# Kernel tuning notes

Hardware: AMD Instinct MI355X
Metric: run time of the kernel (lower is better)

## Reference

```python
import jax, jax.numpy as jnp
import numpy as np

B, N = 128, 64
HID, MLP, DS, DV = 128, 128, 32, 32
DH = MLP - DS - DV  # 64
FILL = -10.0


def _embed_mask(x, W, b, fill):
    # Linear+ReLU on non-NaN rows; fill NaN rows with `fill` (matches embed_with_masking).
    nan = jnp.isnan(x).any(-1)
    e = jax.nn.relu(jnp.where(jnp.isnan(x), 0.0, x) @ W + b)
    return jnp.where(nan[..., None], jnp.asarray(fill, x.dtype), e)


def setup_inputs() -> dict:
    key = jax.random.key(0)
    ks = jax.random.split(key, 12)
    s = 0.05
    return {
        "hidden_states": jax.random.normal(ks[0], (B, N, HID), jnp.float32),
        "obs1": jax.random.normal(ks[1], (B, N, 2), jnp.float32),
        "obs2": jax.random.normal(ks[2], (B, N, 2), jnp.float32),
        "w_sp": jax.random.normal(ks[3], (2, DS), jnp.float32) * s,
        "b_sp": jnp.zeros((DS,), jnp.float32),
        "w_vel": jax.random.normal(ks[4], (2, DV), jnp.float32) * s,
        "b_vel": jnp.zeros((DV,), jnp.float32),
        "w_hid": jax.random.normal(ks[5], (HID, DH), jnp.float32) * s,
        "b_hid": jnp.zeros((DH,), jnp.float32),
        "wq": jax.random.normal(ks[6], (MLP, MLP), jnp.float32) * s,
        "wk": jax.random.normal(ks[7], (MLP, MLP), jnp.float32) * s,
        "wv": jax.random.normal(ks[8], (MLP, MLP), jnp.float32) * s,
        "in_proj_w": jax.random.normal(ks[9], (MLP, 3 * MLP), jnp.float32) * s,
        "in_proj_b": jnp.zeros((3 * MLP,), jnp.float32),
        "mha_out_w": jax.random.normal(ks[10], (MLP, MLP), jnp.float32) * s,
        "mha_out_b": jnp.zeros((MLP,), jnp.float32),
        "out_w": jax.random.normal(ks[11], (MLP, MLP), jnp.float32) * s,
        "out_b": jnp.zeros((MLP,), jnp.float32),
    }


def reference(hidden_states, obs1, obs2, w_sp, b_sp, w_vel, b_vel, w_hid, b_hid,
              wq, wk, wv, in_proj_w, in_proj_b, mha_out_w, mha_out_b, out_w, out_b):
    b, n = obs2.shape[0], obs2.shape[1]
    # relative positions: rel[b,i,j] = obs2[b,j] - obs2[b,i]
    rel = obs2[:, None, :, :] - obs2[:, :, None, :]              # [B,N,N,2]
    sp = _embed_mask(rel, w_sp, b_sp, FILL)                      # [B,N,N,DS]
    hid = _embed_mask(hidden_states, w_hid, b_hid, 0.0)          # [B,N,DH]
    hid_unf = jnp.broadcast_to(hid[:, None, :, :], (b, n, n, DH))
    vel = obs2 - obs1
    relvel = vel[:, None, :, :] - vel[:, :, None, :]             # [B,N,N,2]
    dv = _embed_mask(relvel * 4, w_vel, b_vel, FILL)             # [B,N,N,DV]
    emb = jnp.concatenate([sp, hid_unf, dv], axis=-1)            # [B,N,N,MLP]

    # MHA (1 head) in-proj weights split (stored as [in,out])
    w_iq, w_ik, w_iv = in_proj_w[:, :MLP], in_proj_w[:, MLP:2 * MLP], in_proj_w[:, 2 * MLP:]
    b_iq, b_ik, b_iv = in_proj_b[:MLP], in_proj_b[MLP:2 * MLP], in_proj_b[2 * MLP:]

    # Only the diagonal query position is kept by the final eye-mask gather,
    # and softmax rows are independent, so compute q only at j == i.
    idx = jnp.arange(n)
    emb_diag = emb[:, idx, idx]                                  # [B,N,MLP]
    q = (emb_diag @ wq) @ w_iq + b_iq                            # [B,N,MLP]
    k = (emb @ wk) @ w_ik + b_ik                                 # [B,N,N,MLP]
    v = (emb @ wv) @ w_iv + b_iv                                 # [B,N,N,MLP]

    scores = jnp.einsum('bid,bijd->bij', q, k) / jnp.sqrt(jnp.asarray(MLP, q.dtype))
    attn = jax.nn.softmax(scores, axis=-1)                       # [B,N,N]
    ctx = jnp.einsum('bij,bijd->bid', attn, v)                   # [B,N,MLP]
    mha_out = ctx @ mha_out_w + mha_out_b
    out = mha_out @ out_w + out_b                                # [B,N,out_dim]
    return out.reshape(b * n, -1)
```

## Files before the change

kernel.cpp:

```cpp
#include <hip/hip_runtime.h>

typedef float v2f __attribute__((ext_vector_type(2)));
#define PKFMA(a,b,c) __builtin_elementwise_fma((a),(b),(c))
#define PKMAX(a,b)   __builtin_elementwise_max((a),(b))
static __device__ __forceinline__ v2f vsplat(float s) { return (v2f){s, s}; }
static __device__ __forceinline__ v2f vmk(float a, float b) { return (v2f){a, b}; }
static __device__ __forceinline__ v2f shfl_xor_v2(v2f x, int m) {
    double d = __builtin_bit_cast(double, x);
    d = __shfl_xor(d, m, 64);
    return __builtin_bit_cast(v2f, d);
}

#define WS_WQC   0
#define WS_WKC   16384
#define WS_WVC   32768
#define WS_MOW   49152
#define WS_GQ    65536
#define WS_G0Q   73728
#define WS_FALL  73856
#define WS_FB    90240
#define WS_HID   90368
#define WS_NEED_HID_BYTES ((size_t)(90368 + 128*64*64) * 4)

__global__ __launch_bounds__(256) void precompute1(
    const float* __restrict__ wq, const float* __restrict__ wk,
    const float* __restrict__ wv, const float* __restrict__ in_proj_w,
    const float* __restrict__ mha_out_w, const float* __restrict__ out_w,
    const float* __restrict__ hs, const float* __restrict__ w_hid,
    const float* __restrict__ b_hid, float* __restrict__ ws)
{
    __shared__ __align__(16) float sbuf[4224];
    const int tid = threadIdx.x;

    if (blockIdx.x < 256) {
        const int mat  = blockIdx.x >> 6;
        const int rp   = blockIdx.x & 63;
        const int rsel = tid >> 7;
        const int col  = tid & 127;
        const int r    = 2 * rp + rsel;
        const float* A; const float* Bm; int ldb; float* C;
        if (mat == 0)      { A = wq;        Bm = in_proj_w;       ldb = 384; C = ws + WS_WQC; }
        else if (mat == 1) { A = wk;        Bm = in_proj_w + 128; ldb = 384; C = ws + WS_WKC; }
        else if (mat == 2) { A = wv;        Bm = in_proj_w + 256; ldb = 384; C = ws + WS_WVC; }
        else               { A = mha_out_w; Bm = out_w;           ldb = 128; C = ws + WS_MOW; }
        sbuf[tid] = A[r * 128 + col];
        __syncthreads();
        float acc = 0.f;
        #pragma unroll 8
        for (int d = 0; d < 128; ++d) acc = fmaf(sbuf[rsel * 128 + d], Bm[d * ldb + col], acc);
        C[r * 128 + col] = acc;
    } else {
        const int b2 = blockIdx.x - 256;
        const int b = b2 >> 1, half = b2 & 1;
        const float4* src = (const float4*)(hs + b * 8192 + half * 4096);
        for (int k = tid; k < 1024; k += 256) {
            const int row = k >> 5, c = k & 31;
            *(float4*)&sbuf[row * 132 + 4 * c] = src[k];
        }
        __syncthreads();
        const int ty = tid >> 4, tx = tid & 15;
        float a0c[4] = {0,0,0,0}, a1c[4] = {0,0,0,0};
        for (int d0 = 0; d0 < 128; d0 += 4) {
            const float4 a0 = *(const float4*)&sbuf[(2*ty+0)*132 + d0];
            const float4 a1 = *(const float4*)&sbuf[(2*ty+1)*132 + d0];
            const float* a0p = (const float*)&a0;
            const float* a1p = (const float*)&a1;
            #pragma unroll
            for (int dd = 0; dd < 4; ++dd) {
                const float4 w4 = *(const float4*)&w_hid[(d0+dd)*64 + 4*tx];
                a0c[0] = fmaf(a0p[dd], w4.x, a0c[0]); a0c[1] = fmaf(a0p[dd], w4.y, a0c[1]);
                a0c[2] = fmaf(a0p[dd], w4.z, a0c[2]); a0c[3] = fmaf(a0p[dd], w4.w, a0c[3]);
                a1c[0] = fmaf(a1p[dd], w4.x, a1c[0]); a1c[1] = fmaf(a1p[dd], w4.y, a1c[1]);
                a1c[2] = fmaf(a1p[dd], w4.z, a1c[2]); a1c[3] = fmaf(a1p[dd], w4.w, a1c[3]);
            }
        }
        const float4 bh = *(const float4*)&b_hid[4*tx];
        float* dst = ws + WS_HID + b * 4096 + (32*half + 2*ty) * 64 + 4*tx;
        *(float4*)dst        = make_float4(fmaxf(a0c[0]+bh.x,0.f), fmaxf(a0c[1]+bh.y,0.f),
                                           fmaxf(a0c[2]+bh.z,0.f), fmaxf(a0c[3]+bh.w,0.f));
        *(float4*)(dst + 64) = make_float4(fmaxf(a1c[0]+bh.x,0.f), fmaxf(a1c[1]+bh.y,0.f),
                                           fmaxf(a1c[2]+bh.z,0.f), fmaxf(a1c[3]+bh.w,0.f));
    }
}

__global__ __launch_bounds__(128) void precompute2(
    const float* __restrict__ b_sp, const float* __restrict__ b_vel,
    const float* __restrict__ in_proj_b, const float* __restrict__ mha_out_b,
    const float* __restrict__ out_w, const float* __restrict__ out_b,
    float* __restrict__ ws)
{
    const float* Wqc = ws + WS_WQC;
    const float* Wkc = ws + WS_WKC;
    const float* Wvc = ws + WS_WVC;
    const float* Mow = ws + WS_MOW;
    const int bid = blockIdx.x, tid = threadIdx.x;
    __shared__ __align__(16) float sa[128];

    if (bid < 64) {
        const int k = bid;
        sa[tid] = Wqc[(32 + k) * 128 + tid];
        __syncthreads();
        const int j = tid;
        const int pj = (j < 64) ? 32 + j : ((j < 96) ? j - 64 : j);
        const float* brow = Wkc + pj * 128;
        float acc = 0.f;
        #pragma unroll 8
        for (int d = 0; d < 128; d += 4) {
            const float4 a4 = *(const float4*)&sa[d];
            const float4 b4 = *(const float4*)&brow[d];
            acc = fmaf(a4.x, b4.x, fmaf(a4.y, b4.y, fmaf(a4.z, b4.z, fmaf(a4.w, b4.w, acc))));
        }
        ws[WS_GQ + k * 128 + j] = acc;
    } else if (bid < 192) {
        const int k2 = bid - 64;
        const int srcRow = (k2 < 32) ? k2 : ((k2 < 64) ? 96 + (k2 - 32) : 32 + (k2 - 64));
        sa[tid] = Wvc[srcRow * 128 + tid];
        __syncthreads();
        float acc = 0.f;
        #pragma unroll 8
        for (int m = 0; m < 128; ++m) acc = fmaf(sa[m], Mow[m * 128 + tid], acc);
        ws[WS_FALL + k2 * 128 + tid] = acc;
    } else if (bid == 192) {
        float acc = out_b[tid];
        #pragma unroll 8
        for (int m = 0; m < 128; ++m) {
            acc = fmaf(in_proj_b[256 + m], Mow[m * 128 + tid], acc);
            acc = fmaf(mha_out_b[m], out_w[m * 128 + tid], acc);
        }
        ws[WS_FB + tid] = acc;
    } else {
        float qc = in_proj_b[tid];
        #pragma unroll 4
        for (int s = 0; s < 32; ++s) {
            qc = fmaf(fmaxf(b_sp[s], 0.f),  Wqc[s * 128 + tid], qc);
            qc = fmaf(fmaxf(b_vel[s], 0.f), Wqc[(96 + s) * 128 + tid], qc);
        }
        sa[tid] = qc;
        __syncthreads();
        const int j = tid;
        const int pj = (j < 64) ? 32 + j : ((j < 96) ? j - 64 : j);
        const float* brow = Wkc + pj * 128;
        float acc = 0.f;
        #pragma unroll 8
        for (int d = 0; d < 128; d += 4) {
            const float4 a4 = *(const float4*)&sa[d];
            const float4 b4 = *(const float4*)&brow[d];
            acc = fmaf(a4.x, b4.x, fmaf(a4.y, b4.y, fmaf(a4.z, b4.z, fmaf(a4.w, b4.w, acc))));
        }
        ws[WS_G0Q + j] = acc;
    }
}

#define L_OBS  4224
#define L_WV   4480

template <bool HIDWS>
__global__ __launch_bounds__(256) void attn_main(
    const float* __restrict__ hs, const float* __restrict__ obs1,
    const float* __restrict__ obs2,
    const float* __restrict__ w_sp, const float* __restrict__ b_sp,
    const float* __restrict__ w_vel, const float* __restrict__ b_vel,
    const float* __restrict__ w_hid, const float* __restrict__ b_hid,
    const float* __restrict__ ws, float* __restrict__ out)
{
    const int tid = threadIdx.x;
    const int l   = tid & 63;
    const int w   = tid >> 6;
    const int b   = blockIdx.x >> 2;
    const int i0  = (blockIdx.x & 3) * 16;
    const int rg0 = i0 + 4 * w;

    const float* GQ   = ws + WS_GQ;
    const float* g0q  = ws + WS_G0Q;
    const float* Fall = ws + WS_FALL;
    const float* fbv  = ws + WS_FB;

    __shared__ __align__(16) float smem[7552];
    float* const s_hid = smem;
    float* const s_obs = smem + L_OBS;
    float* const tt = smem + L_WV + w * 768;
    float* const qq = smem + L_WV + w * 768 + 256;
    float* const aa = smem + L_WV + w * 768 + 512;

    if (tid < 64) {
        const int g = b * 64 + tid;
        const float2 o2 = ((const float2*)obs2)[g];
        const float2 o1 = ((const float2*)obs1)[g];
        *(float4*)&s_obs[tid * 4] = make_float4(o2.x, o2.y, o2.x - o1.x, o2.y - o1.y);
    }
    if (HIDWS) {
        const float4* src = (const float4*)(ws + WS_HID + b * 4096);
        #pragma unroll
        for (int k = tid; k < 1024; k += 256) {
            const int row = k >> 4, c4 = (k & 15) * 4;
            const float4 v = src[k];
            *(v2f*)&s_hid[row * 66 + c4]     = vmk(v.x, v.y);
            *(v2f*)&s_hid[row * 66 + c4 + 2] = vmk(v.z, v.w);
        }
    } else {
        const int r = tid >> 2, qseg = (tid & 3) * 16;
        float acc[16];
        #pragma unroll
        for (int c = 0; c < 16; ++c) acc[c] = b_hid[qseg + c];
        for (int k = 0; k < 128; ++k) {
            const float a = hs[b * 8192 + r * 128 + k];
            #pragma unroll
            for (int c4 = 0; c4 < 4; ++c4) {
                const float4 w4 = *(const float4*)&w_hid[k * 64 + qseg + 4 * c4];
                acc[4*c4+0] = fmaf(a, w4.x, acc[4*c4+0]);
                acc[4*c4+1] = fmaf(a, w4.y, acc[4*c4+1]);
                acc[4*c4+2] = fmaf(a, w4.z, acc[4*c4+2]);
                acc[4*c4+3] = fmaf(a, w4.w, acc[4*c4+3]);
            }
        }
        #pragma unroll
        for (int c = 0; c < 16; c += 2)
            *(v2f*)&s_hid[r * 66 + qseg + c] =
                vmk(fmaxf(acc[c], 0.f), fmaxf(acc[c+1], 0.f));
    }
    __syncthreads();

    {
        const v2f bias = *(const v2f*)&g0q[2 * l];
        v2f acc0 = bias, acc1 = bias, acc2 = bias, acc3 = bias;
        for (int k0 = 0; k0 < 64; k0 += 2) {
            const v2f g0 = *(const v2f*)&GQ[k0 * 128 + 2 * l];
            const v2f g1 = *(const v2f*)&GQ[(k0 + 1) * 128 + 2 * l];
            const v2f h0 = *(const v2f*)&s_hid[(rg0 + 0) * 66 + k0];
            const v2f h1 = *(const v2f*)&s_hid[(rg0 + 1) * 66 + k0];
            const v2f h2 = *(const v2f*)&s_hid[(rg0 + 2) * 66 + k0];
            const v2f h3 = *(const v2f*)&s_hid[(rg0 + 3) * 66 + k0];
            acc0 = PKFMA(vsplat(h0.x), g0, PKFMA(vsplat(h0.y), g1, acc0));
            acc1 = PKFMA(vsplat(h1.x), g0, PKFMA(vsplat(h1.y), g1, acc1));
            acc2 = PKFMA(vsplat(h2.x), g0, PKFMA(vsplat(h2.y), g1, acc2));
            acc3 = PKFMA(vsplat(h3.x), g0, PKFMA(vsplat(h3.y), g1, acc3));
        }
        if (l < 32) {
            const int c = 2 * l;
            *(v2f*)&tt[0 * 64 + c] = acc0;  *(v2f*)&tt[1 * 64 + c] = acc1;
            *(v2f*)&tt[2 * 64 + c] = acc2;  *(v2f*)&tt[3 * 64 + c] = acc3;
        } else {
            const int c = 2 * l - 64;
            *(v2f*)&qq[0 * 64 + c] = acc0;  *(v2f*)&qq[1 * 64 + c] = acc1;
            *(v2f*)&qq[2 * 64 + c] = acc2;  *(v2f*)&qq[3 * 64 + c] = acc3;
        }
    }

    float sc[4];
    {
        v2f s0 = (v2f){0.f,0.f}, s1 = s0, s2 = s0, s3 = s0;
        const float* hl = &s_hid[l * 66];
        for (int c0 = 0; c0 < 64; c0 += 2) {
            const v2f h2 = *(const v2f*)&hl[c0];
            s0 = PKFMA(*(const v2f*)&tt[0 * 64 + c0], h2, s0);
            s1 = PKFMA(*(const v2f*)&tt[1 * 64 + c0], h2, s1);
            s2 = PKFMA(*(const v2f*)&tt[2 * 64 + c0], h2, s2);
            s3 = PKFMA(*(const v2f*)&tt[3 * 64 + c0], h2, s3);
        }
        sc[0] = s0.x + s0.y; sc[1] = s1.x + s1.y;
        sc[2] = s2.x + s2.y; sc[3] = s3.x + s3.y;
    }

    {
        const float4 oj = *(const float4*)&s_obs[4 * l];
        float rx[4], ry[4], dx[4], dy[4];
        #pragma unroll
        for (int r = 0; r < 4; ++r) {
            const float4 oi = *(const float4*)&s_obs[4 * (rg0 + r)];
            rx[r] = oj.x - oi.x;  ry[r] = oj.y - oi.y;
            dx[r] = (oj.z - oi.z) * 4.f;  dy[r] = (oj.w - oi.w) * 4.f;
        }
        v2f acc[4] = {{0,0},{0,0},{0,0},{0,0}};
        for (int s0 = 0; s0 < 32; s0 += 2) {
            const v2f w0p = *(const v2f*)&w_sp[s0];
            const v2f w1p = *(const v2f*)&w_sp[32 + s0];
            const v2f bsp = *(const v2f*)&b_sp[s0];
            const v2f u0p = *(const v2f*)&w_vel[s0];
            const v2f u1p = *(const v2f*)&w_vel[32 + s0];
            const v2f bvp = *(const v2f*)&b_vel[s0];
            #pragma unroll
            for (int r = 0; r < 4; ++r) {
                const v2f qs2 = *(const v2f*)&qq[r * 64 + s0];
                const v2f qd2 = *(const v2f*)&qq[r * 64 + 32 + s0];
                const v2f esp = PKMAX(PKFMA(vsplat(rx[r]), w0p,
                                     PKFMA(vsplat(ry[r]), w1p, bsp)), vsplat(0.f));
                acc[r] = PKFMA(qs2, esp, acc[r]);
                const v2f edv = PKMAX(PKFMA(vsplat(dx[r]), u0p,
                                     PKFMA(vsplat(dy[r]), u1p, bvp)), vsplat(0.f));
                acc[r] = PKFMA(qd2, edv, acc[r]);
            }
        }
        const float scale = 0.08838834764831845f;
        v2f p01 = vmk((sc[0] + acc[0].x + acc[0].y) * scale,
                      (sc[1] + acc[1].x + acc[1].y) * scale);
        v2f p23 = vmk((sc[2] + acc[2].x + acc[2].y) * scale,
                      (sc[3] + acc[3].x + acc[3].y) * scale);
        v2f m01 = p01, m23 = p23;
        #pragma unroll
        for (int off = 32; off > 0; off >>= 1) {
            m01 = PKMAX(m01, shfl_xor_v2(m01, off));
            m23 = PKMAX(m23, shfl_xor_v2(m23, off));
        }
        v2f e01 = vmk(__expf(p01.x - m01.x), __expf(p01.y - m01.y));
        v2f e23 = vmk(__expf(p23.x - m23.x), __expf(p23.y - m23.y));
        v2f u01 = e01, u23 = e23;
        #pragma unroll
        for (int off = 32; off > 0; off >>= 1) {
            u01 = u01 + shfl_xor_v2(u01, off);
            u23 = u23 + shfl_xor_v2(u23, off);
        }
        *(float4*)&aa[4 * l] = make_float4(e01.x / u01.x, e01.y / u01.y,
                                           e23.x / u23.x, e23.y / u23.y);
    }

    {
        const int r = l >> 4, s = l & 15;
        const v2f w0p = vmk(w_sp[s],        w_sp[s + 16]);
        const v2f w1p = vmk(w_sp[32 + s],   w_sp[48 + s]);
        const v2f bsp = vmk(b_sp[s],        b_sp[s + 16]);
        const v2f u0p = vmk(w_vel[s],       w_vel[s + 16]);
        const v2f u1p = vmk(w_vel[32 + s],  w_vel[48 + s]);
        const v2f bvp = vmk(b_vel[s],       b_vel[s + 16]);
        const float4 oi = *(const float4*)&s_obs[4 * (rg0 + r)];
        v2f asp = (v2f){0.f, 0.f}, adv = asp;
        for (int j = 0; j < 64; ++j) {
            const float a = aa[4 * j + r];
            const float4 o4 = *(const float4*)&s_obs[4 * j];
            const float rxx = o4.x - oi.x, ryy = o4.y - oi.y;
            const float dxx = (o4.z - oi.z) * 4.f, dyy = (o4.w - oi.w) * 4.f;
            const v2f esp = PKMAX(PKFMA(vsplat(rxx), w0p,
                                 PKFMA(vsplat(ryy), w1p, bsp)), vsplat(0.f));
            asp = PKFMA(vsplat(a), esp, asp);
            const v2f edv = PKMAX(PKFMA(vsplat(dxx), u0p,
                                 PKFMA(vsplat(dyy), u1p, bvp)), vsplat(0.f));
            adv = PKFMA(vsplat(a), edv, adv);
        }
        tt[r * 64 + s]      = asp.x;
        tt[r * 64 + s + 16] = asp.y;
        tt[r * 64 + 32 + s] = adv.x;
        tt[r * 64 + 48 + s] = adv.y;
    }

    {
        float ah0 = 0.f, ah1 = 0.f, ah2 = 0.f, ah3 = 0.f;
        for (int j = 0; j < 64; j += 2) {
            const float4 a0 = *(const float4*)&aa[4 * j];
            const float4 a1 = *(const float4*)&aa[4 * j + 4];
            const float h0 = s_hid[j * 66 + l];
            const float h1 = s_hid[(j + 1) * 66 + l];
            ah0 = fmaf(a0.x, h0, fmaf(a1.x, h1, ah0));
            ah1 = fmaf(a0.y, h0, fmaf(a1.y, h1, ah1));
            ah2 = fmaf(a0.z, h0, fmaf(a1.z, h1, ah2));
            ah3 = fmaf(a0.w, h0, fmaf(a1.w, h1, ah3));
        }
        qq[0 * 64 + l] = ah0;  qq[1 * 64 + l] = ah1;
        qq[2 * 64 + l] = ah2;  qq[3 * 64 + l] = ah3;
    }

    {
        const v2f fb2 = *(const v2f*)&fbv[2 * l];
        v2f o0 = fb2, o1 = fb2, o2 = fb2, o3 = fb2;
        for (int k = 0; k < 64; k += 2) {
            const v2f f0 = *(const v2f*)&Fall[k * 128 + 2 * l];
            const v2f f1 = *(const v2f*)&Fall[(k + 1) * 128 + 2 * l];
            const v2f A0 = *(const v2f*)&tt[0 * 64 + k];
            const v2f A1 = *(const v2f*)&tt[1 * 64 + k];
            const v2f A2 = *(const v2f*)&tt[2 * 64 + k];
            const v2f A3 = *(const v2f*)&tt[3 * 64 + k];
            o0 = PKFMA(vsplat(A0.x), f0, PKFMA(vsplat(A0.y), f1, o0));
            o1 = PKFMA(vsplat(A1.x), f0, PKFMA(vsplat(A1.y), f1, o1));
            o2 = PKFMA(vsplat(A2.x), f0, PKFMA(vsplat(A2.y), f1, o2));
            o3 = PKFMA(vsplat(A3.x), f0, PKFMA(vsplat(A3.y), f1, o3));
        }
        for (int k = 0; k < 64; k += 2) {
            const v2f f0 = *(const v2f*)&Fall[(64 + k) * 128 + 2 * l];
            const v2f f1 = *(const v2f*)&Fall[(65 + k) * 128 + 2 * l];
            const v2f A0 = *(const v2f*)&qq[0 * 64 + k];
            const v2f A1 = *(const v2f*)&qq[1 * 64 + k];
            const v2f A2 = *(const v2f*)&qq[2 * 64 + k];
            const v2f A3 = *(const v2f*)&qq[3 * 64 + k];
            o0 = PKFMA(vsplat(A0.x), f0, PKFMA(vsplat(A0.y), f1, o0));
            o1 = PKFMA(vsplat(A1.x), f0, PKFMA(vsplat(A1.y), f1, o1));
            o2 = PKFMA(vsplat(A2.x), f0, PKFMA(vsplat(A2.y), f1, o2));
            o3 = PKFMA(vsplat(A3.x), f0, PKFMA(vsplat(A3.y), f1, o3));
        }
        const int gr = (b * 64 + rg0) * 128 + 2 * l;
        *(v2f*)&out[gr]           = o0;
        *(v2f*)&out[gr + 128]     = o1;
        *(v2f*)&out[gr + 256]     = o2;
        *(v2f*)&out[gr + 384]     = o3;
    }
}

extern "C" void kernel_launch(void* const* d_in, const int* in_sizes, int n_in,
                              void* d_out, int out_size, void* d_ws, size_t ws_size,
                              hipStream_t stream) {
    const float* hs        = (const float*)d_in[0];
    const float* obs1      = (const float*)d_in[1];
    const float* obs2      = (const float*)d_in[2];
    const float* w_sp      = (const float*)d_in[3];
    const float* b_sp      = (const float*)d_in[4];
    const float* w_vel     = (const float*)d_in[5];
    const float* b_vel     = (const float*)d_in[6];
    const float* w_hid     = (const float*)d_in[7];
    const float* b_hid     = (const float*)d_in[8];
    const float* wq        = (const float*)d_in[9];
    const float* wk        = (const float*)d_in[10];
    const float* wv        = (const float*)d_in[11];
    const float* in_proj_w = (const float*)d_in[12];
    const float* in_proj_b = (const float*)d_in[13];
    const float* mha_out_w = (const float*)d_in[14];
    const float* mha_out_b = (const float*)d_in[15];
    const float* out_w     = (const float*)d_in[16];
    const float* out_b     = (const float*)d_in[17];
    float* ws  = (float*)d_ws;
    float* out = (float*)d_out;

    const bool hidws = (ws_size >= WS_NEED_HID_BYTES);

    precompute1<<<hidws ? 512 : 256, 256, 0, stream>>>(
        wq, wk, wv, in_proj_w, mha_out_w, out_w, hs, w_hid, b_hid, ws);
    precompute2<<<194, 128, 0, stream>>>(
        b_sp, b_vel, in_proj_b, mha_out_b, out_w, out_b, ws);
    if (hidws) {
        attn_main<true><<<512, 256, 0, stream>>>(hs, obs1, obs2, w_sp, b_sp, w_vel, b_vel,
                                                 w_hid, b_hid, ws, out);
    } else {
        attn_main<false><<<512, 256, 0, stream>>>(hs, obs1, obs2, w_sp, b_sp, w_vel, b_vel,
                                                  w_hid, b_hid, ws, out);
    }
}
```

Baseline: 130.5 us.

## Stage precomputed weight matrices in LDS and double block size

The attention kernel now copies the precomputed GQ, g0q, Fall and fb weight tables (about 97 KB) from the workspace into shared memory at block start, and reads them from LDS instead of global memory in the inner loops. Blocks grow to 512 threads covering 32 query rows each, with half as many blocks, so each staged copy is reused by twice as many rows. The hidden-embedding fallback path is re-partitioned across the larger block. The large LDS footprint limits occupancy to roughly one block per CU, and the 256-block grid may leave CUs underused.

```diff
diff --git a/kernel.cpp b/kernel.cpp
--- a/kernel.cpp
+++ b/kernel.cpp
@@ -151,11 +151,17 @@
     }
 }
 
-#define L_OBS  4224
-#define L_WV   4480
+#define L_GQ   0
+#define L_G0Q  8192
+#define L_FALL 8320
+#define L_FB   24704
+#define L_HID  24832
+#define L_OBS  29056
+#define L_WV   29312
+#define L_TOT  35456
 
 template <bool HIDWS>
-__global__ __launch_bounds__(256) void attn_main(
+__global__ __launch_bounds__(512) void attn_main(
     const float* __restrict__ hs, const float* __restrict__ obs1,
     const float* __restrict__ obs2,
     const float* __restrict__ w_sp, const float* __restrict__ b_sp,
@@ -166,22 +172,26 @@
     const int tid = threadIdx.x;
     const int l   = tid & 63;
     const int w   = tid >> 6;
-    const int b   = blockIdx.x >> 2;
-    const int i0  = (blockIdx.x & 3) * 16;
-    const int rg0 = i0 + 4 * w;
-
-    const float* GQ   = ws + WS_GQ;
-    const float* g0q  = ws + WS_G0Q;
-    const float* Fall = ws + WS_FALL;
-    const float* fbv  = ws + WS_FB;
-
-    __shared__ __align__(16) float smem[7552];
-    float* const s_hid = smem;
+    const int b   = blockIdx.x >> 1;
+    const int rg0 = (blockIdx.x & 1) * 32 + 4 * w;
+
+    __shared__ __align__(16) float smem[L_TOT];
+    float* const s_gq  = smem + L_GQ;
+    float* const s_g0q = smem + L_G0Q;
+    float* const s_fall= smem + L_FALL;
+    float* const s_fb  = smem + L_FB;
+    float* const s_hid = smem + L_HID;
     float* const s_obs = smem + L_OBS;
     float* const tt = smem + L_WV + w * 768;
     float* const qq = smem + L_WV + w * 768 + 256;
     float* const aa = smem + L_WV + w * 768 + 512;
 
+    {
+        const float4* src = (const float4*)(ws + WS_GQ);
+        float4* dst = (float4*)smem;
+        #pragma unroll
+        for (int k = tid; k < 6208; k += 512) dst[k] = src[k];
+    }
     if (tid < 64) {
         const int g = b * 64 + tid;
         const float2 o2 = ((const float2*)obs2)[g];
@@ -191,21 +201,21 @@
     if (HIDWS) {
         const float4* src = (const float4*)(ws + WS_HID + b * 4096);
         #pragma unroll
-        for (int k = tid; k < 1024; k += 256) {
+        for (int k = tid; k < 1024; k += 512) {
             const int row = k >> 4, c4 = (k & 15) * 4;
             const float4 v = src[k];
             *(v2f*)&s_hid[row * 66 + c4]     = vmk(v.x, v.y);
             *(v2f*)&s_hid[row * 66 + c4 + 2] = vmk(v.z, v.w);
         }
     } else {
-        const int r = tid >> 2, qseg = (tid & 3) * 16;
-        float acc[16];
-        #pragma unroll
-        for (int c = 0; c < 16; ++c) acc[c] = b_hid[qseg + c];
+        const int r = tid >> 3, qseg = (tid & 7) * 8;
+        float acc[8];
+        #pragma unroll
+        for (int c = 0; c < 8; ++c) acc[c] = b_hid[qseg + c];
         for (int k = 0; k < 128; ++k) {
             const float a = hs[b * 8192 + r * 128 + k];
             #pragma unroll
-            for (int c4 = 0; c4 < 4; ++c4) {
+            for (int c4 = 0; c4 < 2; ++c4) {
                 const float4 w4 = *(const float4*)&w_hid[k * 64 + qseg + 4 * c4];
                 acc[4*c4+0] = fmaf(a, w4.x, acc[4*c4+0]);
                 acc[4*c4+1] = fmaf(a, w4.y, acc[4*c4+1]);
@@ -214,18 +224,18 @@
             }
         }
         #pragma unroll
-        for (int c = 0; c < 16; c += 2)
+        for (int c = 0; c < 8; c += 2)
             *(v2f*)&s_hid[r * 66 + qseg + c] =
                 vmk(fmaxf(acc[c], 0.f), fmaxf(acc[c+1], 0.f));
     }
     __syncthreads();
 
     {
-        const v2f bias = *(const v2f*)&g0q[2 * l];
+        const v2f bias = *(const v2f*)&s_g0q[2 * l];
         v2f acc0 = bias, acc1 = bias, acc2 = bias, acc3 = bias;
         for (int k0 = 0; k0 < 64; k0 += 2) {
-            const v2f g0 = *(const v2f*)&GQ[k0 * 128 + 2 * l];
-            const v2f g1 = *(const v2f*)&GQ[(k0 + 1) * 128 + 2 * l];
+            const v2f g0 = *(const v2f*)&s_gq[k0 * 128 + 2 * l];
+            const v2f g1 = *(const v2f*)&s_gq[(k0 + 1) * 128 + 2 * l];
             const v2f h0 = *(const v2f*)&s_hid[(rg0 + 0) * 66 + k0];
             const v2f h1 = *(const v2f*)&s_hid[(rg0 + 1) * 66 + k0];
             const v2f h2 = *(const v2f*)&s_hid[(rg0 + 2) * 66 + k0];
@@ -358,11 +368,11 @@
     }
 
     {
-        const v2f fb2 = *(const v2f*)&fbv[2 * l];
+        const v2f fb2 = *(const v2f*)&s_fb[2 * l];
         v2f o0 = fb2, o1 = fb2, o2 = fb2, o3 = fb2;
         for (int k = 0; k < 64; k += 2) {
-            const v2f f0 = *(const v2f*)&Fall[k * 128 + 2 * l];
-            const v2f f1 = *(const v2f*)&Fall[(k + 1) * 128 + 2 * l];
+            const v2f f0 = *(const v2f*)&s_fall[k * 128 + 2 * l];
+            const v2f f1 = *(const v2f*)&s_fall[(k + 1) * 128 + 2 * l];
             const v2f A0 = *(const v2f*)&tt[0 * 64 + k];
             const v2f A1 = *(const v2f*)&tt[1 * 64 + k];
             const v2f A2 = *(const v2f*)&tt[2 * 64 + k];
@@ -373,8 +383,8 @@
             o3 = PKFMA(vsplat(A3.x), f0, PKFMA(vsplat(A3.y), f1, o3));
         }
         for (int k = 0; k < 64; k += 2) {
-            const v2f f0 = *(const v2f*)&Fall[(64 + k) * 128 + 2 * l];
-            const v2f f1 = *(const v2f*)&Fall[(65 + k) * 128 + 2 * l];
+            const v2f f0 = *(const v2f*)&s_fall[(64 + k) * 128 + 2 * l];
+            const v2f f1 = *(const v2f*)&s_fall[(65 + k) * 128 + 2 * l];
             const v2f A0 = *(const v2f*)&qq[0 * 64 + k];
             const v2f A1 = *(const v2f*)&qq[1 * 64 + k];
             const v2f A2 = *(const v2f*)&qq[2 * 64 + k];
@@ -423,10 +433,10 @@
     precompute2<<<194, 128, 0, stream>>>(
         b_sp, b_vel, in_proj_b, mha_out_b, out_w, out_b, ws);
     if (hidws) {
-        attn_main<true><<<512, 256, 0, stream>>>(hs, obs1, obs2, w_sp, b_sp, w_vel, b_vel,
+        attn_main<true><<<256, 512, 0, stream>>>(hs, obs1, obs2, w_sp, b_sp, w_vel, b_vel,
                                                  w_hid, b_hid, ws, out);
     } else {
-        attn_main<false><<<512, 256, 0, stream>>>(hs, obs1, obs2, w_sp, b_sp, w_vel, b_vel,
+        attn_main<false><<<256, 512, 0, stream>>>(hs, obs1, obs2, w_sp, b_sp, w_vel, b_vel,
                                                   w_hid, b_hid, ws, out);
     }
 }
```

Result: faster. 125.8 us (-3.5%).
